# Optimization experiments

Hardware: AMD Instinct MI355X
Metric: run time of the kernel (lower is better)

## Reference

```python
import jax, jax.numpy as jnp
import numpy as np

B, N, E = 2, 2048, 1024
H = 16
D = E // H  # head dim = 64


def setup_inputs() -> dict:
    key = jax.random.key(0)
    ks = jax.random.split(key, 11)
    s = 1.0 / np.sqrt(E)
    return {
        "q": jax.random.normal(ks[0], (B, N, E), jnp.float32),
        "k": jax.random.normal(ks[1], (B, N, E), jnp.float32),
        "v": jax.random.normal(ks[2], (B, N, E), jnp.float32),
        "Wq": jax.random.normal(ks[3], (E, E), jnp.float32) * s,
        "bq": jnp.zeros((E,), jnp.float32),
        "Wk": jax.random.normal(ks[4], (E, E), jnp.float32) * s,
        "bk": jnp.zeros((E,), jnp.float32),
        "Wv": jax.random.normal(ks[5], (E, E), jnp.float32) * s,
        "bv": jnp.zeros((E,), jnp.float32),
        "Wo": jax.random.normal(ks[6], (E, E), jnp.float32) * s,
        "bo": jnp.zeros((E,), jnp.float32),
    }


def reference(q, k, v, Wq, bq, Wk, bk, Wv, bv, Wo, bo):
    # projections (torch Linear: x @ W^T + b)
    qp = q @ Wq.T + bq  # [B,N,E]
    kp = k @ Wk.T + bk
    vp = v @ Wv.T + bv
    # separate heads -> [B,H,N,D]
    qh = qp.reshape(B, N, H, D).transpose(0, 2, 1, 3)
    kh = kp.reshape(B, N, H, D).transpose(0, 2, 1, 3)
    vh = vp.reshape(B, N, H, D).transpose(0, 2, 1, 3)
    # scaled dot-product attention, full score matrix like the original
    scale = 1.0 / jnp.sqrt(jnp.asarray(D, qh.dtype))
    attn = jnp.einsum('bhqd,bhkd->bhqk', qh, kh) * scale
    attn = jax.nn.softmax(attn, axis=-1)
    out = jnp.einsum('bhqk,bhkd->bhqd', attn, vh)  # [B,H,N,D]
    # recombine heads
    out = out.transpose(0, 2, 1, 3).reshape(B, N, E)
    return out @ Wo.T + bo
```

## Files before the change

kernel.cpp:

```cpp
#include <hip/hip_runtime.h>

typedef _Float16 f16;
typedef __attribute__((ext_vector_type(2))) _Float16 f16x2;
typedef __attribute__((ext_vector_type(4))) _Float16 f16x4;
typedef __attribute__((ext_vector_type(8))) _Float16 f16x8;
typedef __attribute__((ext_vector_type(4))) float    f32x4;
typedef __attribute__((ext_vector_type(16))) float   f32x16;
typedef __attribute__((ext_vector_type(4))) unsigned u32x4;

static constexpr int B_ = 2, N_ = 2048, E_ = 1024, H_ = 16, D_ = 64;
static constexpr int M_ = B_ * N_;

#define MFMA16(a, b, c) __builtin_amdgcn_mfma_f32_16x16x32_f16(a, b, c, 0, 0, 0)
#define MFMA32(a, b, c) __builtin_amdgcn_mfma_f32_32x32x16_f16(a, b, c, 0, 0, 0)

#define QSCALE 0.18033688011112042f

__device__ __forceinline__ void gload_lds16(const f16* g, f16* l) {
    typedef __attribute__((address_space(1))) const unsigned gu32;
    typedef __attribute__((address_space(3))) unsigned       lu32;
    __builtin_amdgcn_global_load_lds((gu32*)g, (lu32*)l, 16, 0, 0);
}

__global__ __launch_bounds__(256) void cast_all(
    const float* __restrict__ Wq, const float* __restrict__ Wk,
    const float* __restrict__ Wv, const float* __restrict__ Wo,
    const float* __restrict__ q, const float* __restrict__ k,
    const float* __restrict__ v, f16* __restrict__ dst)
{
    const int i = (blockIdx.x * 256 + threadIdx.x) * 4;
    const float* s;
    int j;
    if (i < 4 * E_ * E_) {
        const int which = i >> 20;
        s = (which == 0) ? Wq : (which == 1) ? Wk : (which == 2) ? Wv : Wo;
        j = i & (E_ * E_ - 1);
    } else {
        const int t = i - 4 * E_ * E_;
        const int which = t >> 22;
        s = (which == 0) ? q : (which == 1) ? k : v;
        j = t & (M_ * E_ - 1);
    }
    const f32x4 f = *(const f32x4*)&s[j];
    f16x4 o;
    o[0] = (f16)f[0]; o[1] = (f16)f[1]; o[2] = (f16)f[2]; o[3] = (f16)f[3];
    *(f16x4*)&dst[i] = o;
}

__global__ __launch_bounds__(256) void proj_gemm(
    const f16* __restrict__ Aall, const f16* __restrict__ Wb,
    const float* __restrict__ bq, const float* __restrict__ bk, const float* __restrict__ bv,
    f16* __restrict__ qh, f16* __restrict__ kh, f16* __restrict__ vt)
{
    const int bid  = blockIdx.x;
    const int lin  = (bid & 7) * 96 + (bid >> 3);
    const int z    = lin >> 8;
    const int rem  = lin & 255;
    const int m0   = (rem >> 3) * 128;
    const int n0   = (rem & 7) * 128;

    const f16* A    = Aall + (size_t)z * M_ * E_;
    const f16* W    = Wb + (size_t)z * E_ * E_;
    const float* bias = (z == 0) ? bq : (z == 1) ? bk : bv;

    __shared__ f16 As[128][32];
    __shared__ f16 Bs[128][32];

    const int tid  = threadIdx.x;
    const int lane = tid & 63, w = tid >> 6;
    const int lr = lane & 15, lg = lane >> 4;
    const int wm = (w >> 1) * 64, wn = (w & 1) * 64;

    const int gch = ((lane & 3) ^ ((lane >> 3) & 3)) * 8;
    const f16* ag = A + (size_t)(m0 + w * 32 + (lane >> 2)) * E_ + gch;
    const f16* bg = W + (size_t)(n0 + w * 32 + (lane >> 2)) * E_ + gch;
    f16* al0 = &As[w * 32][0];
    f16* al1 = &As[w * 32 + 16][0];
    f16* bl0 = &Bs[w * 32][0];
    f16* bl1 = &Bs[w * 32 + 16][0];

    const int ca = (lg ^ ((lr >> 1) & 3)) * 8;

    f32x4 acc[4][4];
#pragma unroll
    for (int i = 0; i < 4; i++)
#pragma unroll
        for (int j = 0; j < 4; j++) acc[i][j] = (f32x4){0.f, 0.f, 0.f, 0.f};

    for (int t = 0; t < E_ / 32; ++t) {
        __syncthreads();
        gload_lds16(ag,                 al0);
        gload_lds16(ag + 16 * E_,       al1);
        gload_lds16(bg,                 bl0);
        gload_lds16(bg + 16 * E_,       bl1);
        ag += 32; bg += 32;
        __syncthreads();

        f16x8 af[4], bfr[4];
#pragma unroll
        for (int ms = 0; ms < 4; ms++) af[ms]  = *(const f16x8*)&As[wm + ms * 16 + lr][ca];
#pragma unroll
        for (int ns = 0; ns < 4; ns++) bfr[ns] = *(const f16x8*)&Bs[wn + ns * 16 + lr][ca];
        __builtin_amdgcn_s_setprio(1);
#pragma unroll
        for (int ms = 0; ms < 4; ms++)
#pragma unroll
            for (int ns = 0; ns < 4; ns++)
                acc[ms][ns] = MFMA16(af[ms], bfr[ns], acc[ms][ns]);
        __builtin_amdgcn_s_setprio(0);
    }

    const float oscale = (z == 0) ? QSCALE : 1.0f;
#pragma unroll
    for (int ms = 0; ms < 4; ms++) {
        const int mbase = m0 + wm + ms * 16 + lg * 4;
#pragma unroll
        for (int ns = 0; ns < 4; ns++) {
            const int n  = n0 + wn + ns * 16 + lr;
            const float bn = bias[n];
            const int hh = n >> 6, dd = n & 63;
#pragma unroll
            for (int r = 0; r < 4; r++) {
                const float val = (acc[ms][ns][r] + bn) * oscale;
                const int mm = mbase + r;
                const int bb = mm >> 11;
                const int nn = mm & (N_ - 1);
                if (z == 2) {
                    vt[((size_t)(bb * H_ + hh) * D_ + dd) * N_ + nn] = (f16)val;
                } else {
                    f16* dst = (z == 0) ? qh : kh;
                    dst[((size_t)(bb * H_ + hh) * N_ + nn) * D_ + dd] = (f16)val;
                }
            }
        }
    }
}

__global__ __launch_bounds__(256) void attn_kernel(
    const f16* __restrict__ qh, const f16* __restrict__ kh,
    const f16* __restrict__ vt, f16* __restrict__ ao)
{
    const int bid = blockIdx.x;
    const int swz = (bid & 7) * 64 + (bid >> 3);
    const int qt = swz & 15;
    const int bh = swz >> 4;

    const int tid = threadIdx.x;
    const int w = tid >> 6, lane = tid & 63;
    const int l31 = lane & 31;
    const bool hi = (lane >> 5) != 0;
    const int hib = hi ? 1 : 0;

    const f16* qp = qh + (size_t)bh * N_ * D_;
    const f16* kp = kh + (size_t)bh * N_ * D_;
    const f16* vp = vt + (size_t)bh * D_ * N_;

    const int qrow = qt * 128 + w * 32 + l31;

    f16x8 qf[4];
#pragma unroll
    for (int ks = 0; ks < 4; ks++)
        qf[ks] = *(const f16x8*)&qp[(size_t)qrow * D_ + ks * 16 + hib * 8];

    __shared__ f16 Ks[2][64][64];
    __shared__ f16 Vs[2][64][64];

    const int srow = tid >> 3;
    const int sch  = tid & 7;
    const int ssl  = (sch ^ (srow & 7)) * 8;

    const f16* kg0 = kp + (size_t)srow * D_ + sch * 8;
    const f16* kg1 = kg0 + (size_t)32 * D_;
    const f16* vg0 = vp + (size_t)srow * N_ + sch * 8;
    const f16* vg1 = vg0 + (size_t)32 * N_;

    f32x16 oT0 = {0.f,0.f,0.f,0.f,0.f,0.f,0.f,0.f,0.f,0.f,0.f,0.f,0.f,0.f,0.f,0.f};
    f32x16 oT1 = oT0;
    float mrun = -3.0e38f, lrun = 0.f;

    f16x8 kr0 = *(const f16x8*)(kg0);
    f16x8 kr1 = *(const f16x8*)(kg1);
    f16x8 vr0 = *(const f16x8*)(vg0);
    f16x8 vr1 = *(const f16x8*)(vg1);

    constexpr int NT = N_ / 64;
    int cur = 0;

    for (int t = 0; t < NT; ++t) {
        *(f16x8*)&Ks[cur][srow     ][ssl] = kr0;
        *(f16x8*)&Ks[cur][srow + 32][ssl] = kr1;
        *(f16x8*)&Vs[cur][srow     ][ssl] = vr0;
        *(f16x8*)&Vs[cur][srow + 32][ssl] = vr1;
        if (t + 1 < NT) {
            kr0 = *(const f16x8*)(kg0 + (size_t)(t + 1) * 64 * D_);
            kr1 = *(const f16x8*)(kg1 + (size_t)(t + 1) * 64 * D_);
            vr0 = *(const f16x8*)(vg0 + (t + 1) * 64);
            vr1 = *(const f16x8*)(vg1 + (t + 1) * 64);
        }
        __syncthreads();

        f32x16 sA = {0.f,0.f,0.f,0.f,0.f,0.f,0.f,0.f,0.f,0.f,0.f,0.f,0.f,0.f,0.f,0.f};
        f32x16 sB = sA;
        __builtin_amdgcn_s_setprio(1);
#pragma unroll
        for (int ks = 0; ks < 4; ks++) {
            const int c = (ks * 2 + hib) ^ (l31 & 7);
            const f16x8 kfA = *(const f16x8*)&Ks[cur][l31     ][c * 8];
            const f16x8 kfB = *(const f16x8*)&Ks[cur][l31 + 32][c * 8];
            sA = MFMA32(kfA, qf[ks], sA);
            sB = MFMA32(kfB, qf[ks], sB);
        }
        __builtin_amdgcn_s_setprio(0);

        float tt[16];
#pragma unroll
        for (int r = 0; r < 16; r++) tt[r] = fmaxf(sA[r], sB[r]);
#pragma unroll
        for (int d = 8; d >= 1; d >>= 1)
#pragma unroll
            for (int r = 0; r < d; r++) tt[r] = fmaxf(tt[r], tt[r + d]);
        float pmax = fmaxf(tt[0], __shfl_xor(tt[0], 32));

        if (!__all(pmax - mrun <= 8.0f)) {
            const float mnew = fmaxf(mrun, pmax);
            const float alpha = __builtin_amdgcn_exp2f(mrun - mnew);
            mrun = mnew;
            lrun *= alpha;
#pragma unroll
            for (int r = 0; r < 16; r++) { oT0[r] *= alpha; oT1[r] *= alpha; }
        }

        float p0 = 0.f, p1 = 0.f, p2 = 0.f, p3 = 0.f;
#pragma unroll
        for (int r = 0; r < 16; r += 4) {
            sA[r]   = __builtin_amdgcn_exp2f(sA[r]   - mrun); p0 += sA[r];
            sA[r+1] = __builtin_amdgcn_exp2f(sA[r+1] - mrun); p1 += sA[r+1];
            sA[r+2] = __builtin_amdgcn_exp2f(sA[r+2] - mrun); p2 += sA[r+2];
            sA[r+3] = __builtin_amdgcn_exp2f(sA[r+3] - mrun); p3 += sA[r+3];
        }
#pragma unroll
        for (int r = 0; r < 16; r += 4) {
            sB[r]   = __builtin_amdgcn_exp2f(sB[r]   - mrun); p0 += sB[r];
            sB[r+1] = __builtin_amdgcn_exp2f(sB[r+1] - mrun); p1 += sB[r+1];
            sB[r+2] = __builtin_amdgcn_exp2f(sB[r+2] - mrun); p2 += sB[r+2];
            sB[r+3] = __builtin_amdgcn_exp2f(sB[r+3] - mrun); p3 += sB[r+3];
        }
        float lsum = (p0 + p1) + (p2 + p3);
        lsum += __shfl_xor(lsum, 32);
        lrun += lsum;

        __builtin_amdgcn_s_setprio(1);
#define PVSTEP(PP0,PP1,PP2,PP3,PP4,PP5,PP6,PP7, KSI)                                   \
        {                                                                              \
            const unsigned w0 = __builtin_bit_cast(unsigned, __builtin_amdgcn_cvt_pkrtz(PP0, PP1)); \
            const unsigned w1 = __builtin_bit_cast(unsigned, __builtin_amdgcn_cvt_pkrtz(PP2, PP3)); \
            const unsigned w2 = __builtin_bit_cast(unsigned, __builtin_amdgcn_cvt_pkrtz(PP4, PP5)); \
            const unsigned w3 = __builtin_bit_cast(unsigned, __builtin_amdgcn_cvt_pkrtz(PP6, PP7)); \
            const unsigned x0 = (unsigned)__shfl_xor((int)w0, 32);                     \
            const unsigned x1 = (unsigned)__shfl_xor((int)w1, 32);                     \
            const unsigned x2 = (unsigned)__shfl_xor((int)w2, 32);                     \
            const unsigned x3 = (unsigned)__shfl_xor((int)w3, 32);                     \
            u32x4 pw;                                                                  \
            pw[0] = hi ? x2 : w0;                                                      \
            pw[1] = hi ? x3 : w1;                                                      \
            pw[2] = hi ? w2 : x0;                                                      \
            pw[3] = hi ? w3 : x1;                                                      \
            const f16x8 pa = __builtin_bit_cast(f16x8, pw);                            \
            const int c = ((KSI) * 2 + hib) ^ (l31 & 7);                               \
            const f16x8 vf0 = *(const f16x8*)&Vs[cur][l31     ][c * 8];                \
            const f16x8 vf1 = *(const f16x8*)&Vs[cur][l31 + 32][c * 8];                \
            oT0 = MFMA32(vf0, pa, oT0);                                                \
            oT1 = MFMA32(vf1, pa, oT1);                                                \
        }
        PVSTEP(sA[0],sA[1],sA[2],sA[3],sA[4],sA[5],sA[6],sA[7], 0)
        PVSTEP(sA[8],sA[9],sA[10],sA[11],sA[12],sA[13],sA[14],sA[15], 1)
        PVSTEP(sB[0],sB[1],sB[2],sB[3],sB[4],sB[5],sB[6],sB[7], 2)
        PVSTEP(sB[8],sB[9],sB[10],sB[11],sB[12],sB[13],sB[14],sB[15], 3)
#undef PVSTEP
        __builtin_amdgcn_s_setprio(0);

        cur ^= 1;
    }

    const float inv = 1.0f / lrun;
    const int b = bh >> 4, h = bh & 15;
    f16* dst = ao + (size_t)(b * N_ + qrow) * E_ + h * 64 + hib * 4;
#pragma unroll
    for (int g = 0; g < 4; g++) {
        f16x4 o0, o1;
#pragma unroll
        for (int j = 0; j < 4; j++) {
            o0[j] = (f16)(oT0[g * 4 + j] * inv);
            o1[j] = (f16)(oT1[g * 4 + j] * inv);
        }
        *(f16x4*)&dst[8 * g]      = o0;
        *(f16x4*)&dst[8 * g + 32] = o1;
    }
}

__global__ __launch_bounds__(256) void out_gemm(
    const f16* __restrict__ ao, const f16* __restrict__ Wo,
    const float* __restrict__ bo, float* __restrict__ out)
{
    __shared__ f16 As[128][32];
    __shared__ f16 Bs[128][32];

    const int bid = blockIdx.x;
    const int lin = (bid & 7) * 32 + (bid >> 3);
    const int m0  = (lin >> 3) * 128;
    const int n0  = (lin & 7) * 128;

    const int tid  = threadIdx.x;
    const int lane = tid & 63, w = tid >> 6;
    const int lr = lane & 15, lg = lane >> 4;
    const int wm = (w >> 1) * 64, wn = (w & 1) * 64;

    const int gch = ((lane & 3) ^ ((lane >> 3) & 3)) * 8;
    const f16* ag = ao + (size_t)(m0 + w * 32 + (lane >> 2)) * E_ + gch;
    const f16* bg = Wo + (size_t)(n0 + w * 32 + (lane >> 2)) * E_ + gch;
    f16* al0 = &As[w * 32][0];
    f16* al1 = &As[w * 32 + 16][0];
    f16* bl0 = &Bs[w * 32][0];
    f16* bl1 = &Bs[w * 32 + 16][0];

    const int ca = (lg ^ ((lr >> 1) & 3)) * 8;

    f32x4 acc[4][4];
#pragma unroll
    for (int i = 0; i < 4; i++)
#pragma unroll
        for (int j = 0; j < 4; j++) acc[i][j] = (f32x4){0.f, 0.f, 0.f, 0.f};

    for (int t = 0; t < E_ / 32; ++t) {
        __syncthreads();
        gload_lds16(ag,            al0);
        gload_lds16(ag + 16 * E_,  al1);
        gload_lds16(bg,            bl0);
        gload_lds16(bg + 16 * E_,  bl1);
        ag += 32; bg += 32;
        __syncthreads();

        f16x8 af[4], bfr[4];
#pragma unroll
        for (int ms = 0; ms < 4; ms++) af[ms]  = *(const f16x8*)&As[wm + ms * 16 + lr][ca];
#pragma unroll
        for (int ns = 0; ns < 4; ns++) bfr[ns] = *(const f16x8*)&Bs[wn + ns * 16 + lr][ca];
        __builtin_amdgcn_s_setprio(1);
#pragma unroll
        for (int ms = 0; ms < 4; ms++)
#pragma unroll
            for (int ns = 0; ns < 4; ns++)
                acc[ms][ns] = MFMA16(af[ms], bfr[ns], acc[ms][ns]);
        __builtin_amdgcn_s_setprio(0);
    }

#pragma unroll
    for (int ms = 0; ms < 4; ms++) {
        const int mbase = m0 + wm + ms * 16 + lg * 4;
#pragma unroll
        for (int ns = 0; ns < 4; ns++) {
            const int n = n0 + wn + ns * 16 + lr;
            const float bn = bo[n];
#pragma unroll
            for (int r = 0; r < 4; r++) {
                out[(size_t)(mbase + r) * E_ + n] = acc[ms][ns][r] + bn;
            }
        }
    }
}

extern "C" void kernel_launch(void* const* d_in, const int* in_sizes, int n_in,
                              void* d_out, int out_size, void* d_ws, size_t ws_size,
                              hipStream_t stream) {
    const float* q  = (const float*)d_in[0];
    const float* k  = (const float*)d_in[1];
    const float* v  = (const float*)d_in[2];
    const float* Wq = (const float*)d_in[3];
    const float* bq = (const float*)d_in[4];
    const float* Wk = (const float*)d_in[5];
    const float* bk = (const float*)d_in[6];
    const float* Wv = (const float*)d_in[7];
    const float* bv = (const float*)d_in[8];
    const float* Wo = (const float*)d_in[9];
    const float* bo = (const float*)d_in[10];
    float* out = (float*)d_out;

    char* ws = (char*)d_ws;
    f16* cast = (f16*)ws;
    f16* Wb   = cast;
    f16* Aall = cast + (size_t)4 * E_ * E_;
    f16* qh = (f16*)(ws + (size_t)32 * 1024 * 1024);
    f16* kh = (f16*)(ws + (size_t)40 * 1024 * 1024);
    f16* vt = (f16*)(ws + (size_t)48 * 1024 * 1024);
    f16* ao = (f16*)(ws + (size_t)56 * 1024 * 1024);

    cast_all<<<16384, 256, 0, stream>>>(Wq, Wk, Wv, Wo, q, k, v, cast);
    proj_gemm<<<768, 256, 0, stream>>>(Aall, Wb, bq, bk, bv, qh, kh, vt);
    attn_kernel<<<512, 256, 0, stream>>>(qh, kh, vt, ao);
    out_gemm<<<256, 256, 0, stream>>>(ao, Wb + (size_t)3 * E_ * E_, bo, out);
}
```

Measured before the change: 149.7 us.

## Fuse fp32-to-fp16 activation cast into projection GEMM A-tile loading

```diff
diff --git a/kernel.cpp b/kernel.cpp
--- a/kernel.cpp
+++ b/kernel.cpp
@@ -22,25 +22,15 @@
     __builtin_amdgcn_global_load_lds((gu32*)g, (lu32*)l, 16, 0, 0);
 }
 
-__global__ __launch_bounds__(256) void cast_all(
+__global__ __launch_bounds__(256) void castw_kernel(
     const float* __restrict__ Wq, const float* __restrict__ Wk,
     const float* __restrict__ Wv, const float* __restrict__ Wo,
-    const float* __restrict__ q, const float* __restrict__ k,
-    const float* __restrict__ v, f16* __restrict__ dst)
+    f16* __restrict__ dst)
 {
     const int i = (blockIdx.x * 256 + threadIdx.x) * 4;
-    const float* s;
-    int j;
-    if (i < 4 * E_ * E_) {
-        const int which = i >> 20;
-        s = (which == 0) ? Wq : (which == 1) ? Wk : (which == 2) ? Wv : Wo;
-        j = i & (E_ * E_ - 1);
-    } else {
-        const int t = i - 4 * E_ * E_;
-        const int which = t >> 22;
-        s = (which == 0) ? q : (which == 1) ? k : v;
-        j = t & (M_ * E_ - 1);
-    }
+    const int which = i >> 20;
+    const float* s = (which == 0) ? Wq : (which == 1) ? Wk : (which == 2) ? Wv : Wo;
+    const int j = i & (E_ * E_ - 1);
     const f32x4 f = *(const f32x4*)&s[j];
     f16x4 o;
     o[0] = (f16)f[0]; o[1] = (f16)f[1]; o[2] = (f16)f[2]; o[3] = (f16)f[3];
@@ -48,7 +38,8 @@
 }
 
 __global__ __launch_bounds__(256) void proj_gemm(
-    const f16* __restrict__ Aall, const f16* __restrict__ Wb,
+    const float* __restrict__ q, const float* __restrict__ k, const float* __restrict__ v,
+    const f16* __restrict__ Wb,
     const float* __restrict__ bq, const float* __restrict__ bk, const float* __restrict__ bv,
     f16* __restrict__ qh, f16* __restrict__ kh, f16* __restrict__ vt)
 {
@@ -59,8 +50,8 @@
     const int m0   = (rem >> 3) * 128;
     const int n0   = (rem & 7) * 128;
 
-    const f16* A    = Aall + (size_t)z * M_ * E_;
-    const f16* W    = Wb + (size_t)z * E_ * E_;
+    const float* A    = (z == 0) ? q  : (z == 1) ? k  : v;
+    const f16*   W    = Wb + (size_t)z * E_ * E_;
     const float* bias = (z == 0) ? bq : (z == 1) ? bk : bv;
 
     __shared__ f16 As[128][32];
@@ -72,35 +63,60 @@
     const int wm = (w >> 1) * 64, wn = (w & 1) * 64;
 
     const int gch = ((lane & 3) ^ ((lane >> 3) & 3)) * 8;
-    const f16* ag = A + (size_t)(m0 + w * 32 + (lane >> 2)) * E_ + gch;
     const f16* bg = W + (size_t)(n0 + w * 32 + (lane >> 2)) * E_ + gch;
-    f16* al0 = &As[w * 32][0];
-    f16* al1 = &As[w * 32 + 16][0];
     f16* bl0 = &Bs[w * 32][0];
     f16* bl1 = &Bs[w * 32 + 16][0];
 
-    const int ca = (lg ^ ((lr >> 1) & 3)) * 8;
+    const int srow = tid >> 1;
+    const int h    = tid & 1;
+    const int s3   = srow & 3;
+    const int c0   = (2 * h)     ^ s3;
+    const int c1   = (2 * h + 1) ^ s3;
+    const float* ag = A + (size_t)(m0 + srow) * E_;
+
+    const int caA = (lg ^ (lr & 3)) * 8;
+    const int caB = (lg ^ ((lr >> 1) & 3)) * 8;
 
     f32x4 acc[4][4];
 #pragma unroll
     for (int i = 0; i < 4; i++)
 #pragma unroll
         for (int j = 0; j < 4; j++) acc[i][j] = (f32x4){0.f, 0.f, 0.f, 0.f};
+
+    f32x4 aA0 = *(const f32x4*)(ag + 8 * c0);
+    f32x4 aA1 = *(const f32x4*)(ag + 8 * c0 + 4);
+    f32x4 aB0 = *(const f32x4*)(ag + 8 * c1);
+    f32x4 aB1 = *(const f32x4*)(ag + 8 * c1 + 4);
 
     for (int t = 0; t < E_ / 32; ++t) {
         __syncthreads();
-        gload_lds16(ag,                 al0);
-        gload_lds16(ag + 16 * E_,       al1);
-        gload_lds16(bg,                 bl0);
-        gload_lds16(bg + 16 * E_,       bl1);
-        ag += 32; bg += 32;
+        gload_lds16(bg,           bl0);
+        gload_lds16(bg + 16 * E_, bl1);
+        bg += 32;
+        {
+            f16x8 w0, w1;
+#pragma unroll
+            for (int j = 0; j < 4; j++) {
+                w0[j] = (f16)aA0[j]; w0[4 + j] = (f16)aA1[j];
+                w1[j] = (f16)aB0[j]; w1[4 + j] = (f16)aB1[j];
+            }
+            *(f16x8*)&As[srow][16 * h]     = w0;
+            *(f16x8*)&As[srow][16 * h + 8] = w1;
+        }
+        if (t + 1 < E_ / 32) {
+            const float* an = ag + (t + 1) * 32;
+            aA0 = *(const f32x4*)(an + 8 * c0);
+            aA1 = *(const f32x4*)(an + 8 * c0 + 4);
+            aB0 = *(const f32x4*)(an + 8 * c1);
+            aB1 = *(const f32x4*)(an + 8 * c1 + 4);
+        }
         __syncthreads();
 
         f16x8 af[4], bfr[4];
 #pragma unroll
-        for (int ms = 0; ms < 4; ms++) af[ms]  = *(const f16x8*)&As[wm + ms * 16 + lr][ca];
-#pragma unroll
-        for (int ns = 0; ns < 4; ns++) bfr[ns] = *(const f16x8*)&Bs[wn + ns * 16 + lr][ca];
+        for (int ms = 0; ms < 4; ms++) af[ms]  = *(const f16x8*)&As[wm + ms * 16 + lr][caA];
+#pragma unroll
+        for (int ns = 0; ns < 4; ns++) bfr[ns] = *(const f16x8*)&Bs[wn + ns * 16 + lr][caB];
         __builtin_amdgcn_s_setprio(1);
 #pragma unroll
         for (int ms = 0; ms < 4; ms++)
@@ -212,14 +228,14 @@
         }
         __builtin_amdgcn_s_setprio(0);
 
-        float tt[16];
-#pragma unroll
-        for (int r = 0; r < 16; r++) tt[r] = fmaxf(sA[r], sB[r]);
+        float t16[16];
+#pragma unroll
+        for (int r = 0; r < 16; r++) t16[r] = fmaxf(sA[r], sB[r]);
 #pragma unroll
         for (int d = 8; d >= 1; d >>= 1)
 #pragma unroll
-            for (int r = 0; r < d; r++) tt[r] = fmaxf(tt[r], tt[r + d]);
-        float pmax = fmaxf(tt[0], __shfl_xor(tt[0], 32));
+            for (int r = 0; r < d; r++) t16[r] = fmaxf(t16[r], t16[r + d]);
+        const float pmax = fmaxf(t16[0], __shfl_xor(t16[0], 32));
 
         if (!__all(pmax - mrun <= 8.0f)) {
             const float mnew = fmaxf(mrun, pmax);
@@ -386,16 +402,14 @@
     float* out = (float*)d_out;
 
     char* ws = (char*)d_ws;
-    f16* cast = (f16*)ws;
-    f16* Wb   = cast;
-    f16* Aall = cast + (size_t)4 * E_ * E_;
+    f16* Wb = (f16*)ws;
     f16* qh = (f16*)(ws + (size_t)32 * 1024 * 1024);
     f16* kh = (f16*)(ws + (size_t)40 * 1024 * 1024);
     f16* vt = (f16*)(ws + (size_t)48 * 1024 * 1024);
     f16* ao = (f16*)(ws + (size_t)56 * 1024 * 1024);
 
-    cast_all<<<16384, 256, 0, stream>>>(Wq, Wk, Wv, Wo, q, k, v, cast);
-    proj_gemm<<<768, 256, 0, stream>>>(Aall, Wb, bq, bk, bv, qh, kh, vt);
+    castw_kernel<<<4096, 256, 0, stream>>>(Wq, Wk, Wv, Wo, Wb);
+    proj_gemm<<<768, 256, 0, stream>>>(q, k, v, Wb, bq, bk, bv, qh, kh, vt);
     attn_kernel<<<512, 256, 0, stream>>>(qh, kh, vt, ao);
     out_gemm<<<256, 256, 0, stream>>>(ao, Wb + (size_t)3 * E_ * E_, bo, out);
 }
```

Measured after the change: 146.1 us. 1.02x faster.
